# Kernel optimization log

Hardware: AMD Instinct MI355X
Metric: run time of the kernel (lower is better)

## Reference

```python
import jax, jax.numpy as jnp
import numpy as np

D_MODEL = 128
NHEAD = 8
DFF = 256
NW = 1024      # number of windows
WIN = 128      # max tokens per window
N_TOTAL = NW * WIN
NEG = -1e9


def _build_indices():
    rng = np.random.RandomState(0)
    cnt = rng.randint(WIN // 2, WIN + 1, size=NW)
    cnt_prv = rng.randint(WIN // 2, WIN + 1, size=NW)
    inds = np.concatenate([w * WIN + np.arange(c) for w, c in enumerate(cnt)]).astype(np.int64)
    inds_prv = np.concatenate([w * WIN + np.arange(c) for w, c in enumerate(cnt_prv)]).astype(np.int64)
    kpm_prv = (np.arange(WIN)[None, :] >= cnt_prv[:, None])  # True = padded key slot
    keep_inds = np.sort(rng.choice(N_TOTAL, len(inds), replace=False)).astype(np.int64)
    keep_inds_prv = np.sort(rng.choice(N_TOTAL, len(inds_prv), replace=False)).astype(np.int64)
    return inds, inds_prv, kpm_prv, keep_inds, keep_inds_prv


def setup_inputs() -> dict:
    inds, inds_prv, kpm_prv, keep_inds, keep_inds_prv = _build_indices()
    key = jax.random.key(0)
    ks = jax.random.split(key, 12)
    f = jnp.float32
    s = 0.05
    d, dff = D_MODEL, DFF
    return {
        'src': jax.random.normal(ks[0], (N_TOTAL, d), f),
        'src_prv': jax.random.normal(ks[1], (N_TOTAL, d), f),
        'pos': jax.random.normal(ks[2], (NW, WIN, d), f),
        'pos_prv': jax.random.normal(ks[3], (NW, WIN, d), f),
        'in_proj_w': jax.random.normal(ks[4], (3 * d, d), f) * s,
        'in_proj_b': jnp.zeros((3 * d,), f),
        'out_proj_w': jax.random.normal(ks[5], (d, d), f) * s,
        'out_proj_b': jnp.zeros((d,), f),
        'lin1_w': jax.random.normal(ks[6], (dff, d), f) * s,
        'lin1_b': jnp.zeros((dff,), f),
        'lin2_w': jax.random.normal(ks[7], (d, dff), f) * s,
        'lin2_b': jnp.zeros((d,), f),
        'ln1_g': jnp.ones((d,), f),
        'ln1_b': jnp.zeros((d,), f),
        'ln2_g': jnp.ones((d,), f),
        'ln2_b': jnp.zeros((d,), f),
        'keep_inds': jnp.asarray(keep_inds),
        'keep_inds_prv': jnp.asarray(keep_inds_prv),
        'inds': jnp.asarray(inds),
        'inds_prv': jnp.asarray(inds_prv),
        'key_padding_mask_prv': jnp.asarray(kpm_prv),
    }


def _layer_norm(x, g, b, eps=1e-5):
    m = x.mean(-1, keepdims=True)
    v = ((x - m) ** 2).mean(-1, keepdims=True)
    return (x - m) / jnp.sqrt(v + eps) * g + b


def reference(src, src_prv, pos, pos_prv, in_proj_w, in_proj_b, out_proj_w, out_proj_b,
              lin1_w, lin1_b, lin2_w, lin2_b, ln1_g, ln1_b, ln2_g, ln2_b,
              keep_inds, keep_inds_prv, inds, inds_prv, key_padding_mask_prv):
    d, h = D_MODEL, NHEAD
    hd = d // h
    # src[keep_inds] gather, then flat2window_v2 scatter into window grid
    sel = src[keep_inds]
    sel_prv = src_prv[keep_inds_prv]
    grid = jnp.zeros((NW * WIN, d), src.dtype).at[inds].set(sel).reshape(NW, WIN, d)
    grid_prv = jnp.zeros((NW * WIN, d), src.dtype).at[inds_prv].set(sel_prv).reshape(NW, WIN, d)
    q = grid + pos
    k = grid_prv + pos_prv
    v = grid_prv
    wq, wk, wv = jnp.split(in_proj_w, 3, axis=0)
    bq, bk, bv = jnp.split(in_proj_b, 3, axis=0)
    qh = (q @ wq.T + bq).reshape(NW, WIN, h, hd)
    kh = (k @ wk.T + bk).reshape(NW, WIN, h, hd)
    vh = (v @ wv.T + bv).reshape(NW, WIN, h, hd)
    scores = jnp.einsum('nqhd,nkhd->nhqk', qh, kh) / np.sqrt(hd).astype(np.float32)
    scores = jnp.where(key_padding_mask_prv[:, None, None, :], NEG, scores)
    attn = jax.nn.softmax(scores, axis=-1)
    out = jnp.einsum('nhqk,nkhd->nqhd', attn, vh).reshape(NW, WIN, d)
    out = out @ out_proj_w.T + out_proj_b
    # window2flat_v2 gather back, residual add at kept positions
    out_sel = out.reshape(NW * WIN, d)[inds]
    src = src.at[keep_inds].add(out_sel)  # dropout1 is identity in eval
    src = _layer_norm(src, ln1_g, ln1_b)
    ff = jax.nn.relu(src @ lin1_w.T + lin1_b) @ lin2_w.T + lin2_b
    src = _layer_norm(src + ff, ln2_g, ln2_b)
    return src
```

## Files before the change

### kernel.cpp

```cpp
#include <hip/hip_runtime.h>

#define NWIN 1024
#define WIN 128
#define DM 128
#define NTOT (NWIN*WIN)

typedef __bf16 bf16;
typedef __bf16 bf16x2 __attribute__((ext_vector_type(2)));
typedef __bf16 bf16x4 __attribute__((ext_vector_type(4)));
typedef __bf16 bf16x8 __attribute__((ext_vector_type(8)));
typedef float f32x4 __attribute__((ext_vector_type(4)));
typedef float f32x16 __attribute__((ext_vector_type(16)));

#define MFMA16(a,b,c) __builtin_amdgcn_mfma_f32_16x16x32_bf16(a,b,c,0,0,0)
#define MFMA32(a,b,c) __builtin_amdgcn_mfma_f32_32x32x16_bf16(a,b,c,0,0,0)

#define QSCALE 0.36067376022224085f


__global__ void k_prep1(const float* __restrict__ inproj, const float* __restrict__ outproj,
                        const float* __restrict__ w1, const float* __restrict__ w2,
                        bf16* __restrict__ whi,
                        int* __restrict__ mq, int* __restrict__ mkv, int* __restrict__ flag) {
    int i = blockIdx.x * 256 + threadIdx.x;
    if (i == 0) *flag = 0;
    float v;
    if (i < 49152)       v = inproj[i];
    else if (i < 65536)  v = outproj[i - 49152];
    else if (i < 98304)  v = w1[i - 65536];
    else                 v = w2[i - 98304];
    if (i < 16384) v *= QSCALE;
    whi[i] = (bf16)v;
    mq[i] = -1; mkv[i] = -1;
}

__global__ void k_prep2(const int* __restrict__ kpm_i, int* __restrict__ flag,
                        const int* __restrict__ inds, const int* __restrict__ keep, int n,
                        const int* __restrict__ inds_p, const int* __restrict__ keep_p, int np,
                        int* __restrict__ mq, int* __restrict__ mkv) {
    int j = blockIdx.x * 256 + threadIdx.x;
    if (j < 32768) {
        int v = kpm_i[j];
        if (v != 0 && v != 1) atomicOr(flag, 1);
    }
    if (j < n)  mq[inds[j]]    = keep[j];
    if (j < np) mkv[inds_p[j]] = keep_p[j];
}

__global__ void k_prep3(const int* __restrict__ kpm_i, const unsigned char* __restrict__ kpm_b,
                        const int* __restrict__ flag, unsigned char* __restrict__ kmask,
                        const float4* __restrict__ s, float4* __restrict__ d, int n4) {
    int i = blockIdx.x * 256 + threadIdx.x;
    if (i < 131072) {
        int byte_mode = *flag;
        kmask[i] = byte_mode ? (kpm_b[i] != 0) : (kpm_i[i] != 0);
    }
    int stride = gridDim.x * 256;
    for (int k = i; k < n4; k += stride) d[k] = s[k];
}

__device__ __forceinline__ void proj1p(const bf16* __restrict__ Xh,
                                       const bf16* __restrict__ WH,
                                       int l15, int g16, f32x4 acc[8]) {
    #pragma unroll
    for (int ks = 0; ks < 4; ks++) {
        bf16x8 ah = *(const bf16x8*)(Xh + l15 * 136 + ks*32 + g16*8);
        #pragma unroll
        for (int tn = 0; tn < 8; tn++) {
            bf16x8 bh = *(const bf16x8*)(WH + (size_t)(16*tn + l15) * DM + ks*32 + g16*8);
            acc[tn] = MFMA16(ah, bh, acc[tn]);
        }
    }
}

__global__ __launch_bounds__(256, 4) void k_qkv(
    const float* __restrict__ src, const float* __restrict__ src_prv,
    const float* __restrict__ pos, const float* __restrict__ pos_prv,
    const bf16* __restrict__ whi,
    const float* __restrict__ bqkv,
    const int* __restrict__ mq, const int* __restrict__ mkv,
    bf16* __restrict__ Qg, bf16* __restrict__ Kg, bf16* __restrict__ Vtg)
{
    const int blk = blockIdx.x;
    const int role = blockIdx.y;
    const int rbase = blk * 64;
    const int w = blk >> 1;
    const int kb = (blk & 1) * 64;
    const int tid = threadIdx.x;
    const int lane = tid & 63, wv = tid >> 6;
    const int l15 = lane & 15, g16 = lane >> 4;
    __shared__ bf16 X[64*136];
    __shared__ bf16 Bb[9216];

    const int srow = tid >> 2, sq4 = tid & 3;
    const int p = rbase + srow;

    if (role == 0) {
        const int g = mq[p];
        float4 a[8];
        const float4* pr = (const float4*)(pos + (size_t)p * DM + sq4 * 32);
        #pragma unroll
        for (int i = 0; i < 8; i++) a[i] = pr[i];
        if (g >= 0) {
            const float4* sr = (const float4*)(src + (size_t)g * DM + sq4 * 32);
            #pragma unroll
            for (int i = 0; i < 8; i++) {
                float4 s4 = sr[i];
                a[i].x += s4.x; a[i].y += s4.y; a[i].z += s4.z; a[i].w += s4.w;
            }
        }
        bf16* xh = X + srow * 136 + sq4 * 32;
        #pragma unroll
        for (int i = 0; i < 8; i++) {
            bf16x4 h = { (bf16)a[i].x, (bf16)a[i].y, (bf16)a[i].z, (bf16)a[i].w };
            *(bf16x4*)(xh + i * 4) = h;
        }
    } else {
        const int g = mkv[p];
        float4 a[8];
        if (role == 2) {
            const float4* pr = (const float4*)(pos_prv + (size_t)p * DM + sq4 * 32);
            #pragma unroll
            for (int i = 0; i < 8; i++) a[i] = pr[i];
        } else {
            #pragma unroll
            for (int i = 0; i < 8; i++) a[i] = make_float4(0.f, 0.f, 0.f, 0.f);
        }
        if (g >= 0) {
            const float4* sr = (const float4*)(src_prv + (size_t)g * DM + sq4 * 32);
            #pragma unroll
            for (int i = 0; i < 8; i++) {
                float4 s4 = sr[i];
                a[i].x += s4.x; a[i].y += s4.y; a[i].z += s4.z; a[i].w += s4.w;
            }
        }
        bf16* xh = X + srow * 136 + sq4 * 32;
        #pragma unroll
        for (int i = 0; i < 8; i++) {
            bf16x4 h = { (bf16)a[i].x, (bf16)a[i].y, (bf16)a[i].z, (bf16)a[i].w };
            *(bf16x4*)(xh + i * 4) = h;
        }
    }
    __syncthreads();

    const bf16* W = whi + (role == 0 ? 0 : (role == 1 ? 256*DM : 128*DM));
    f32x4 acc[8];
    for (int tn = 0; tn < 8; tn++) acc[tn] = {};
    proj1p(X + 16*wv*136, W, l15, g16, acc);

    if (role == 1) {
        #pragma unroll
        for (int tn = 0; tn < 8; tn++) {
            float bias = bqkv[256 + 16*tn + l15];
            int dim = 16*tn + l15;
            bf16x4 b = { (bf16)(acc[tn][0] + bias), (bf16)(acc[tn][1] + bias),
                         (bf16)(acc[tn][2] + bias), (bf16)(acc[tn][3] + bias) };
            *(bf16x4*)(Bb + dim * 72 + 16*wv + 4*g16) = b;
        }
        __syncthreads();
        #pragma unroll
        for (int it = 0; it < 4; it++) {
            int c = it * 256 + tid;
            int dim = c >> 3, off = (c & 7) * 8;
            *(bf16x8*)(Vtg + ((size_t)w * 128 + dim) * 128 + kb + off) = *(const bf16x8*)(Bb + dim*72 + off);
        }
    } else {
        const float bsc  = (role == 0) ? QSCALE : 1.f;
        const int   boff = (role == 0) ? 0 : 128;
        #pragma unroll
        for (int tn = 0; tn < 8; tn++) {
            float bias = bqkv[boff + 16*tn + l15] * bsc;
            #pragma unroll
            for (int r = 0; r < 4; r++)
                Bb[(16*wv + 4*g16 + r) * 136 + 16*tn + l15] = (bf16)(acc[tn][r] + bias);
        }
        __syncthreads();
        bf16* dst = (role == 0) ? Qg : Kg;
        #pragma unroll
        for (int it = 0; it < 4; it++) {
            int c = it * 256 + tid;
            int row = c >> 4, off = (c & 15) * 8;
            *(bf16x8*)(dst + (size_t)(rbase + row) * DM + off) = *(const bf16x8*)(Bb + row*136 + off);
        }
    }
}

__global__ __launch_bounds__(256) void k_attn(
    const bf16* __restrict__ Qg, const bf16* __restrict__ Kg, const bf16* __restrict__ Vtg,
    const bf16* __restrict__ whi, const float* __restrict__ ob,
    const unsigned char* __restrict__ kmask, const int* __restrict__ mq,
    float* __restrict__ x1)
{
    const int w = blockIdx.x;
    const int tid = threadIdx.x;
    const int lane = tid & 63, wv = tid >> 6;
    const int l15 = lane & 15, g16 = lane >> 4;
    const int l31 = lane & 31, h32 = lane >> 5;
    __shared__ bf16 P[4][32 * 136];
    bf16* myP = &P[wv][0];

    float mval[4];
    #pragma unroll
    for (int kt = 0; kt < 4; kt++) mval[kt] = kmask[w * WIN + 32*kt + l31] ? -1e9f : 0.f;

    const bf16* Qw = Qg + (size_t)w * WIN * DM;
    const bf16* Kw = Kg + (size_t)w * WIN * DM;
    const bf16* Vw = Vtg + (size_t)w * WIN * DM;

    f32x4 oacc[8][2];
    for (int h = 0; h < 8; h++) { oacc[h][0] = {}; oacc[h][1] = {}; }

    #pragma unroll
    for (int h = 0; h < 8; h++) {
        bf16x8 qf = *(const bf16x8*)(Qw + (size_t)(32*wv + l31) * DM + 16*h + h32*8);
        f32x16 s[4];
        #pragma unroll
        for (int kt = 0; kt < 4; kt++) {
            bf16x8 kf = *(const bf16x8*)(Kw + (size_t)(32*kt + l31) * DM + 16*h + h32*8);
            f32x16 z = {};
            s[kt] = MFMA32(qf, kf, z);
        }
        #pragma unroll
        for (int r = 0; r < 16; r++) {
            float s0 = s[0][r] + mval[0];
            float s1 = s[1][r] + mval[1];
            float s2 = s[2][r] + mval[2];
            float s3 = s[3][r] + mval[3];
            float m = fmaxf(fmaxf(s0, s1), fmaxf(s2, s3));
            #pragma unroll
            for (int d = 1; d <= 16; d <<= 1) m = fmaxf(m, __shfl_xor(m, d));
            float e0 = exp2f(s0 - m), e1 = exp2f(s1 - m);
            float e2 = exp2f(s2 - m), e3 = exp2f(s3 - m);
            float sum = e0 + e1 + e2 + e3;
            #pragma unroll
            for (int d = 1; d <= 16; d <<= 1) sum += __shfl_xor(sum, d);
            float inv = __builtin_amdgcn_rcpf(sum);
            int qrow = (r & 3) + 8 * (r >> 2) + 4 * h32;
            myP[qrow * 136 +      l31] = (bf16)(e0 * inv);
            myP[qrow * 136 + 32 + l31] = (bf16)(e1 * inv);
            myP[qrow * 136 + 64 + l31] = (bf16)(e2 * inv);
            myP[qrow * 136 + 96 + l31] = (bf16)(e3 * inv);
        }
        #pragma unroll
        for (int ks = 0; ks < 4; ks++) {
            bf16x8 p0 = *(const bf16x8*)(myP + (l15     ) * 136 + ks*32 + g16*8);
            bf16x8 p1 = *(const bf16x8*)(myP + (16 + l15) * 136 + ks*32 + g16*8);
            bf16x8 vf = *(const bf16x8*)(Vw + (size_t)(16*h + l15) * DM + ks*32 + g16*8);
            oacc[h][0] = MFMA16(p0, vf, oacc[h][0]);
            oacc[h][1] = MFMA16(p1, vf, oacc[h][1]);
        }
    }

    #pragma unroll
    for (int h = 0; h < 8; h++) {
        #pragma unroll
        for (int tq = 0; tq < 2; tq++) {
            #pragma unroll
            for (int r = 0; r < 4; r++)
                myP[(16*tq + 4*g16 + r) * 136 + 16*h + l15] = (bf16)oacc[h][tq][r];
        }
    }

    const bf16* Woh = whi + 49152;
    f32x4 oc[2][8];
    for (int tq = 0; tq < 2; tq++)
        for (int tn = 0; tn < 8; tn++)
            oc[tq][tn] = {};
    #pragma unroll
    for (int ks = 0; ks < 4; ks++) {
        bf16x8 a0 = *(const bf16x8*)(myP + (l15     ) * 136 + ks*32 + g16*8);
        bf16x8 a1 = *(const bf16x8*)(myP + (16 + l15) * 136 + ks*32 + g16*8);
        #pragma unroll
        for (int tn = 0; tn < 8; tn++) {
            bf16x8 bh = *(const bf16x8*)(Woh + (size_t)(16*tn + l15) * DM + ks*32 + g16*8);
            oc[0][tn] = MFMA16(a0, bh, oc[0][tn]);
            oc[1][tn] = MFMA16(a1, bh, oc[1][tn]);
        }
    }

    float obv[8];
    #pragma unroll
    for (int tn = 0; tn < 8; tn++) obv[tn] = ob[16*tn + l15];
    #pragma unroll
    for (int tq = 0; tq < 2; tq++) {
        #pragma unroll
        for (int r = 0; r < 4; r++) {
            int qrow = 32*wv + 16*tq + 4*g16 + r;
            int g = mq[w * WIN + qrow];
            if (g < 0) continue;
            float* orow = x1 + (size_t)g * DM;
            #pragma unroll
            for (int tn = 0; tn < 8; tn++)
                orow[16*tn + l15] += oc[tq][tn][r] + obv[tn];
        }
    }
}

__global__ __launch_bounds__(256, 4) void k_ffn(
    const float* __restrict__ x1, const bf16* __restrict__ whi,
    const float* __restrict__ g1, const float* __restrict__ b1ln,
    const float* __restrict__ fb1, const float* __restrict__ fb2,
    const float* __restrict__ g2, const float* __restrict__ b2ln,
    float* __restrict__ out)
{
    const int tid = threadIdx.x;
    const int lane = tid & 63, wv = tid >> 6;
    const int l15 = lane & 15, g16 = lane >> 4;
    const int rbase = blockIdx.x * 64 + wv * 16;
    __shared__ bf16 Hb[4][16 * 264];
    bf16* myH = &Hb[wv][0];
    const bf16* W1h = whi + 65536;
    const bf16* W2h = whi + 98304;

    float xv[4][8];
    float sum = 0.f, sq = 0.f;
    const float* xrow = x1 + (size_t)(rbase + l15) * DM;
    #pragma unroll
    for (int ks = 0; ks < 4; ks++) {
        float4 a = *(const float4*)(xrow + ks*32 + g16*8);
        float4 b = *(const float4*)(xrow + ks*32 + g16*8 + 4);
        xv[ks][0]=a.x; xv[ks][1]=a.y; xv[ks][2]=a.z; xv[ks][3]=a.w;
        xv[ks][4]=b.x; xv[ks][5]=b.y; xv[ks][6]=b.z; xv[ks][7]=b.w;
        sum += a.x+a.y+a.z+a.w + b.x+b.y+b.z+b.w;
        sq  += a.x*a.x+a.y*a.y+a.z*a.z+a.w*a.w + b.x*b.x+b.y*b.y+b.z*b.z+b.w*b.w;
    }
    sum += __shfl_xor(sum, 16); sum += __shfl_xor(sum, 32);
    sq  += __shfl_xor(sq, 16);  sq  += __shfl_xor(sq, 32);
    float mean = sum * (1.f/128.f);
    float var  = sq * (1.f/128.f) - mean * mean;
    float rstd = rsqrtf(var + 1e-5f);

    bf16x8 ah[4];
    #pragma unroll
    for (int ks = 0; ks < 4; ks++) {
        #pragma unroll
        for (int j = 0; j < 8; j++) {
            int col = ks*32 + g16*8 + j;
            float y = (xv[ks][j] - mean) * rstd * g1[col] + b1ln[col];
            ah[ks][j] = (bf16)y;
        }
    }

    #pragma unroll
    for (int c = 0; c < 2; c++) {
        f32x4 h1[8];
        #pragma unroll
        for (int t = 0; t < 8; t++) h1[t] = {};
        #pragma unroll
        for (int ks = 0; ks < 4; ks++) {
            #pragma unroll
            for (int t = 0; t < 8; t++) {
                bf16x8 bh = *(const bf16x8*)(W1h + (size_t)(16*(8*c + t) + l15) * DM + ks*32 + g16*8);
                h1[t] = MFMA16(ah[ks], bh, h1[t]);
            }
        }
        #pragma unroll
        for (int t = 0; t < 8; t++) {
            int tn = 8*c + t;
            float bias = fb1[16*tn + l15];
            #pragma unroll
            for (int r = 0; r < 4; r++) {
                float v = fmaxf(h1[t][r] + bias, 0.f);
                myH[(4*g16 + r) * 264 + 16*tn + l15] = (bf16)v;
            }
        }
    }

    f32x4 o[8];
    #pragma unroll
    for (int tn = 0; tn < 8; tn++) o[tn] = {};
    #pragma unroll
    for (int ks = 0; ks < 8; ks++) {
        bf16x8 a = *(const bf16x8*)(myH + l15 * 264 + ks*32 + g16*8);
        #pragma unroll
        for (int tn = 0; tn < 8; tn++) {
            bf16x8 bh = *(const bf16x8*)(W2h + (size_t)(16*tn + l15) * 256 + ks*32 + g16*8);
            o[tn] = MFMA16(a, bh, o[tn]);
        }
    }

    #pragma unroll
    for (int r = 0; r < 4; r++) {
        int rw = 4*g16 + r;
        int row = rbase + rw;
        float bm = __shfl(mean, rw);
        float br = __shfl(rstd, rw);
        float tmp[8];
        float s2 = 0.f, q2 = 0.f;
        #pragma unroll
        for (int tn = 0; tn < 8; tn++) {
            int col = 16*tn + l15;
            float xr = x1[(size_t)row * DM + col];
            float y  = (xr - bm) * br * g1[col] + b1ln[col];
            float v  = o[tn][r] + fb2[col] + y;
            tmp[tn] = v; s2 += v; q2 += v * v;
        }
        #pragma unroll
        for (int d = 1; d <= 8; d <<= 1) { s2 += __shfl_xor(s2, d); q2 += __shfl_xor(q2, d); }
        float mean2 = s2 * (1.f/128.f);
        float var2  = q2 * (1.f/128.f) - mean2 * mean2;
        float rstd2 = rsqrtf(var2 + 1e-5f);
        #pragma unroll
        for (int tn = 0; tn < 8; tn++) {
            int col = 16*tn + l15;
            out[(size_t)row * DM + col] = (tmp[tn] - mean2) * rstd2 * g2[col] + b2ln[col];
        }
    }
}

extern "C" void kernel_launch(void* const* d_in, const int* in_sizes, int n_in,
                              void* d_out, int out_size, void* d_ws, size_t ws_size,
                              hipStream_t stream)
{
    const float* src      = (const float*)d_in[0];
    const float* src_prv  = (const float*)d_in[1];
    const float* pos      = (const float*)d_in[2];
    const float* pos_prv  = (const float*)d_in[3];
    const float* inpw     = (const float*)d_in[4];
    const float* inpb     = (const float*)d_in[5];
    const float* outpw    = (const float*)d_in[6];
    const float* outpb    = (const float*)d_in[7];
    const float* l1w      = (const float*)d_in[8];
    const float* l1b      = (const float*)d_in[9];
    const float* l2w      = (const float*)d_in[10];
    const float* l2b      = (const float*)d_in[11];
    const float* ln1g     = (const float*)d_in[12];
    const float* ln1b     = (const float*)d_in[13];
    const float* ln2g     = (const float*)d_in[14];
    const float* ln2b     = (const float*)d_in[15];
    const int* keep       = (const int*)d_in[16];
    const int* keep_p     = (const int*)d_in[17];
    const int* inds       = (const int*)d_in[18];
    const int* inds_p     = (const int*)d_in[19];
    const int n_inds = in_sizes[18], n_prv = in_sizes[19];

    char* wsb = (char*)d_ws;
    bf16* whi  = (bf16*)(wsb);
    int*  mq   = (int*)(wsb + 524288);
    int*  mkv  = (int*)(wsb + 1048576);
    bf16* Qb   = (bf16*)(wsb + 1572864);
    bf16* Kb   = (bf16*)(wsb + 1572864 + 33554432);
    bf16* Vtb  = (bf16*)(wsb + 1572864 + 2u*33554432);
    unsigned char* kmask = (unsigned char*)(wsb + 1572864 + 3u*33554432);
    int* mflag = (int*)(wsb + 1572864 + 3u*33554432 + 131072);
    float* x1 = (float*)d_out;

    int mmax = n_inds > n_prv ? n_inds : n_prv;
    if (mmax < 32768) mmax = 32768;
    k_prep1<<<512, 256, 0, stream>>>(inpw, outpw, l1w, l2w, whi, mq, mkv, mflag);
    k_prep2<<<(mmax + 255) / 256, 256, 0, stream>>>((const int*)d_in[20], mflag,
                                                    inds, keep, n_inds, inds_p, keep_p, n_prv, mq, mkv);
    k_prep3<<<2048, 256, 0, stream>>>((const int*)d_in[20], (const unsigned char*)d_in[20], mflag, kmask,
                                      (const float4*)src, (float4*)x1, NTOT * DM / 4);
    k_qkv<<<dim3(2048, 3), 256, 0, stream>>>(src, src_prv, pos, pos_prv, whi, inpb, mq, mkv, Qb, Kb, Vtb);
    k_attn<<<NWIN, 256, 0, stream>>>(Qb, Kb, Vtb, whi, outpb, kmask, mq, x1);
    k_ffn<<<NTOT / 64, 256, 0, stream>>>(x1, whi, ln1g, ln1b, l1b, l2b, ln2g, ln2b, (float*)d_out);
}
```

Measured before the change: 456.0 us.

## Replace src copy and scatter-add with bf16 attention output and inverse-index gather in FFN

Instead of copying src into the output buffer and scatter-adding fp32 attention results into it, attention now writes a dense bf16 output tensor per window. The FFN kernel gathers that output through a new inverse index map and adds it to src on the fly. This removes a full fp32 copy pass and the read-modify-write scatter. The qkv kernel also shares one LDS buffer to allow higher occupancy. In exchange the residual is rounded to bf16 and the FFN does extra indirect reads, including an uncoalesced per-element reread in the epilogue.

```diff
diff --git a/kernel.cpp b/kernel.cpp
--- a/kernel.cpp
+++ b/kernel.cpp
@@ -6,7 +6,6 @@
 #define NTOT (NWIN*WIN)
 
 typedef __bf16 bf16;
-typedef __bf16 bf16x2 __attribute__((ext_vector_type(2)));
 typedef __bf16 bf16x4 __attribute__((ext_vector_type(4)));
 typedef __bf16 bf16x8 __attribute__((ext_vector_type(8)));
 typedef float f32x4 __attribute__((ext_vector_type(4)));
@@ -21,7 +20,8 @@
 __global__ void k_prep1(const float* __restrict__ inproj, const float* __restrict__ outproj,
                         const float* __restrict__ w1, const float* __restrict__ w2,
                         bf16* __restrict__ whi,
-                        int* __restrict__ mq, int* __restrict__ mkv, int* __restrict__ flag) {
+                        int* __restrict__ mq, int* __restrict__ mkv, int* __restrict__ im,
+                        int* __restrict__ flag) {
     int i = blockIdx.x * 256 + threadIdx.x;
     if (i == 0) *flag = 0;
     float v;
@@ -31,32 +31,27 @@
     else                 v = w2[i - 98304];
     if (i < 16384) v *= QSCALE;
     whi[i] = (bf16)v;
-    mq[i] = -1; mkv[i] = -1;
+    mq[i] = -1; mkv[i] = -1; im[i] = -1;
 }
 
 __global__ void k_prep2(const int* __restrict__ kpm_i, int* __restrict__ flag,
                         const int* __restrict__ inds, const int* __restrict__ keep, int n,
                         const int* __restrict__ inds_p, const int* __restrict__ keep_p, int np,
-                        int* __restrict__ mq, int* __restrict__ mkv) {
+                        int* __restrict__ mq, int* __restrict__ mkv, int* __restrict__ im) {
     int j = blockIdx.x * 256 + threadIdx.x;
     if (j < 32768) {
         int v = kpm_i[j];
         if (v != 0 && v != 1) atomicOr(flag, 1);
     }
-    if (j < n)  mq[inds[j]]    = keep[j];
+    if (j < n)  { mq[inds[j]] = keep[j]; im[keep[j]] = inds[j]; }
     if (j < np) mkv[inds_p[j]] = keep_p[j];
 }
 
 __global__ void k_prep3(const int* __restrict__ kpm_i, const unsigned char* __restrict__ kpm_b,
-                        const int* __restrict__ flag, unsigned char* __restrict__ kmask,
-                        const float4* __restrict__ s, float4* __restrict__ d, int n4) {
+                        const int* __restrict__ flag, unsigned char* __restrict__ kmask) {
     int i = blockIdx.x * 256 + threadIdx.x;
-    if (i < 131072) {
-        int byte_mode = *flag;
-        kmask[i] = byte_mode ? (kpm_b[i] != 0) : (kpm_i[i] != 0);
-    }
-    int stride = gridDim.x * 256;
-    for (int k = i; k < n4; k += stride) d[k] = s[k];
+    int byte_mode = *flag;
+    kmask[i] = byte_mode ? (kpm_b[i] != 0) : (kpm_i[i] != 0);
 }
 
 __device__ __forceinline__ void proj1p(const bf16* __restrict__ Xh,
@@ -73,7 +68,7 @@
     }
 }
 
-__global__ __launch_bounds__(256, 4) void k_qkv(
+__global__ __launch_bounds__(256, 6) void k_qkv(
     const float* __restrict__ src, const float* __restrict__ src_prv,
     const float* __restrict__ pos, const float* __restrict__ pos_prv,
     const bf16* __restrict__ whi,
@@ -89,64 +84,59 @@
     const int tid = threadIdx.x;
     const int lane = tid & 63, wv = tid >> 6;
     const int l15 = lane & 15, g16 = lane >> 4;
-    __shared__ bf16 X[64*136];
-    __shared__ bf16 Bb[9216];
+    __shared__ bf16 S[9216];
 
     const int srow = tid >> 2, sq4 = tid & 3;
     const int p = rbase + srow;
 
-    if (role == 0) {
-        const int g = mq[p];
+    {
         float4 a[8];
-        const float4* pr = (const float4*)(pos + (size_t)p * DM + sq4 * 32);
-        #pragma unroll
-        for (int i = 0; i < 8; i++) a[i] = pr[i];
-        if (g >= 0) {
-            const float4* sr = (const float4*)(src + (size_t)g * DM + sq4 * 32);
-            #pragma unroll
-            for (int i = 0; i < 8; i++) {
-                float4 s4 = sr[i];
-                a[i].x += s4.x; a[i].y += s4.y; a[i].z += s4.z; a[i].w += s4.w;
+        if (role == 0) {
+            const int g = mq[p];
+            const float4* pr = (const float4*)(pos + (size_t)p * DM + sq4 * 32);
+            #pragma unroll
+            for (int i = 0; i < 8; i++) a[i] = pr[i];
+            if (g >= 0) {
+                const float4* sr = (const float4*)(src + (size_t)g * DM + sq4 * 32);
+                #pragma unroll
+                for (int i = 0; i < 8; i++) {
+                    float4 s4 = sr[i];
+                    a[i].x += s4.x; a[i].y += s4.y; a[i].z += s4.z; a[i].w += s4.w;
+                }
             }
-        }
-        bf16* xh = X + srow * 136 + sq4 * 32;
+        } else {
+            const int g = mkv[p];
+            if (role == 2) {
+                const float4* pr = (const float4*)(pos_prv + (size_t)p * DM + sq4 * 32);
+                #pragma unroll
+                for (int i = 0; i < 8; i++) a[i] = pr[i];
+            } else {
+                #pragma unroll
+                for (int i = 0; i < 8; i++) a[i] = make_float4(0.f, 0.f, 0.f, 0.f);
+            }
+            if (g >= 0) {
+                const float4* sr = (const float4*)(src_prv + (size_t)g * DM + sq4 * 32);
+                #pragma unroll
+                for (int i = 0; i < 8; i++) {
+                    float4 s4 = sr[i];
+                    a[i].x += s4.x; a[i].y += s4.y; a[i].z += s4.z; a[i].w += s4.w;
+                }
+            }
+        }
+        bf16* xh = S + srow * 136 + sq4 * 32;
         #pragma unroll
         for (int i = 0; i < 8; i++) {
             bf16x4 h = { (bf16)a[i].x, (bf16)a[i].y, (bf16)a[i].z, (bf16)a[i].w };
             *(bf16x4*)(xh + i * 4) = h;
         }
-    } else {
-        const int g = mkv[p];
-        float4 a[8];
-        if (role == 2) {
-            const float4* pr = (const float4*)(pos_prv + (size_t)p * DM + sq4 * 32);
-            #pragma unroll
-            for (int i = 0; i < 8; i++) a[i] = pr[i];
-        } else {
-            #pragma unroll
-            for (int i = 0; i < 8; i++) a[i] = make_float4(0.f, 0.f, 0.f, 0.f);
-        }
-        if (g >= 0) {
-            const float4* sr = (const float4*)(src_prv + (size_t)g * DM + sq4 * 32);
-            #pragma unroll
-            for (int i = 0; i < 8; i++) {
-                float4 s4 = sr[i];
-                a[i].x += s4.x; a[i].y += s4.y; a[i].z += s4.z; a[i].w += s4.w;
-            }
-        }
-        bf16* xh = X + srow * 136 + sq4 * 32;
-        #pragma unroll
-        for (int i = 0; i < 8; i++) {
-            bf16x4 h = { (bf16)a[i].x, (bf16)a[i].y, (bf16)a[i].z, (bf16)a[i].w };
-            *(bf16x4*)(xh + i * 4) = h;
-        }
     }
     __syncthreads();
 
     const bf16* W = whi + (role == 0 ? 0 : (role == 1 ? 256*DM : 128*DM));
     f32x4 acc[8];
     for (int tn = 0; tn < 8; tn++) acc[tn] = {};
-    proj1p(X + 16*wv*136, W, l15, g16, acc);
+    proj1p(S + 16*wv*136, W, l15, g16, acc);
+    __syncthreads();
 
     if (role == 1) {
         #pragma unroll
@@ -155,14 +145,14 @@
             int dim = 16*tn + l15;
             bf16x4 b = { (bf16)(acc[tn][0] + bias), (bf16)(acc[tn][1] + bias),
                          (bf16)(acc[tn][2] + bias), (bf16)(acc[tn][3] + bias) };
-            *(bf16x4*)(Bb + dim * 72 + 16*wv + 4*g16) = b;
+            *(bf16x4*)(S + dim * 72 + 16*wv + 4*g16) = b;
         }
         __syncthreads();
         #pragma unroll
         for (int it = 0; it < 4; it++) {
             int c = it * 256 + tid;
             int dim = c >> 3, off = (c & 7) * 8;
-            *(bf16x8*)(Vtg + ((size_t)w * 128 + dim) * 128 + kb + off) = *(const bf16x8*)(Bb + dim*72 + off);
+            *(bf16x8*)(Vtg + ((size_t)w * 128 + dim) * 128 + kb + off) = *(const bf16x8*)(S + dim*72 + off);
         }
     } else {
         const float bsc  = (role == 0) ? QSCALE : 1.f;
@@ -172,7 +162,7 @@
             float bias = bqkv[boff + 16*tn + l15] * bsc;
             #pragma unroll
             for (int r = 0; r < 4; r++)
-                Bb[(16*wv + 4*g16 + r) * 136 + 16*tn + l15] = (bf16)(acc[tn][r] + bias);
+                S[(16*wv + 4*g16 + r) * 136 + 16*tn + l15] = (bf16)(acc[tn][r] + bias);
         }
         __syncthreads();
         bf16* dst = (role == 0) ? Qg : Kg;
@@ -180,7 +170,7 @@
         for (int it = 0; it < 4; it++) {
             int c = it * 256 + tid;
             int row = c >> 4, off = (c & 15) * 8;
-            *(bf16x8*)(dst + (size_t)(rbase + row) * DM + off) = *(const bf16x8*)(Bb + row*136 + off);
+            *(bf16x8*)(dst + (size_t)(rbase + row) * DM + off) = *(const bf16x8*)(S + row*136 + off);
         }
     }
 }
@@ -188,8 +178,8 @@
 __global__ __launch_bounds__(256) void k_attn(
     const bf16* __restrict__ Qg, const bf16* __restrict__ Kg, const bf16* __restrict__ Vtg,
     const bf16* __restrict__ whi, const float* __restrict__ ob,
-    const unsigned char* __restrict__ kmask, const int* __restrict__ mq,
-    float* __restrict__ x1)
+    const unsigned char* __restrict__ kmask,
+    bf16* __restrict__ Ob)
 {
     const int w = blockIdx.x;
     const int tid = threadIdx.x;
@@ -284,20 +274,25 @@
     #pragma unroll
     for (int tq = 0; tq < 2; tq++) {
         #pragma unroll
-        for (int r = 0; r < 4; r++) {
-            int qrow = 32*wv + 16*tq + 4*g16 + r;
-            int g = mq[w * WIN + qrow];
-            if (g < 0) continue;
-            float* orow = x1 + (size_t)g * DM;
-            #pragma unroll
-            for (int tn = 0; tn < 8; tn++)
-                orow[16*tn + l15] += oc[tq][tn][r] + obv[tn];
-        }
+        for (int tn = 0; tn < 8; tn++) {
+            #pragma unroll
+            for (int r = 0; r < 4; r++)
+                myP[(16*tq + 4*g16 + r) * 136 + 16*tn + l15] = (bf16)(oc[tq][tn][r] + obv[tn]);
+        }
+    }
+    __syncthreads();
+    bf16* Orow = Ob + ((size_t)w * 128 + 32*wv) * DM;
+    #pragma unroll
+    for (int it = 0; it < 8; it++) {
+        int c = it * 64 + lane;
+        int row = c >> 4, off = (c & 15) * 8;
+        *(bf16x8*)(Orow + (size_t)row * DM + off) = *(const bf16x8*)(myP + row*136 + off);
     }
 }
 
 __global__ __launch_bounds__(256, 4) void k_ffn(
-    const float* __restrict__ x1, const bf16* __restrict__ whi,
+    const float* __restrict__ src, const bf16* __restrict__ Ob, const int* __restrict__ im,
+    const bf16* __restrict__ whi,
     const float* __restrict__ g1, const float* __restrict__ b1ln,
     const float* __restrict__ fb1, const float* __restrict__ fb2,
     const float* __restrict__ g2, const float* __restrict__ b2ln,
@@ -312,17 +307,25 @@
     const bf16* W1h = whi + 65536;
     const bf16* W2h = whi + 98304;
 
+    const int myrow = rbase + l15;
+    const int imr = im[myrow];
     float xv[4][8];
     float sum = 0.f, sq = 0.f;
-    const float* xrow = x1 + (size_t)(rbase + l15) * DM;
+    const float* xrow = src + (size_t)myrow * DM;
+    const bf16* orow = Ob + (size_t)(imr < 0 ? 0 : imr) * DM;
     #pragma unroll
     for (int ks = 0; ks < 4; ks++) {
         float4 a = *(const float4*)(xrow + ks*32 + g16*8);
         float4 b = *(const float4*)(xrow + ks*32 + g16*8 + 4);
         xv[ks][0]=a.x; xv[ks][1]=a.y; xv[ks][2]=a.z; xv[ks][3]=a.w;
         xv[ks][4]=b.x; xv[ks][5]=b.y; xv[ks][6]=b.z; xv[ks][7]=b.w;
-        sum += a.x+a.y+a.z+a.w + b.x+b.y+b.z+b.w;
-        sq  += a.x*a.x+a.y*a.y+a.z*a.z+a.w*a.w + b.x*b.x+b.y*b.y+b.z*b.z+b.w*b.w;
+        if (imr >= 0) {
+            bf16x8 ov = *(const bf16x8*)(orow + ks*32 + g16*8);
+            #pragma unroll
+            for (int j = 0; j < 8; j++) xv[ks][j] = xv[ks][j] + (float)ov[j];
+        }
+        #pragma unroll
+        for (int j = 0; j < 8; j++) { sum += xv[ks][j]; sq += xv[ks][j]*xv[ks][j]; }
     }
     sum += __shfl_xor(sum, 16); sum += __shfl_xor(sum, 32);
     sq  += __shfl_xor(sq, 16);  sq  += __shfl_xor(sq, 32);
@@ -385,12 +388,14 @@
         int row = rbase + rw;
         float bm = __shfl(mean, rw);
         float br = __shfl(rstd, rw);
+        int imr2 = __shfl(imr, rw);
         float tmp[8];
         float s2 = 0.f, q2 = 0.f;
         #pragma unroll
         for (int tn = 0; tn < 8; tn++) {
             int col = 16*tn + l15;
-            float xr = x1[(size_t)row * DM + col];
+            float xr = src[(size_t)row * DM + col];
+            if (imr2 >= 0) xr = xr + (float)Ob[(size_t)imr2 * DM + col];
             float y  = (xr - bm) * br * g1[col] + b1ln[col];
             float v  = o[tn][r] + fb2[col] + y;
             tmp[tn] = v; s2 += v; q2 += v * v;
@@ -438,21 +443,21 @@
     bf16* whi  = (bf16*)(wsb);
     int*  mq   = (int*)(wsb + 524288);
     int*  mkv  = (int*)(wsb + 1048576);
-    bf16* Qb   = (bf16*)(wsb + 1572864);
-    bf16* Kb   = (bf16*)(wsb + 1572864 + 33554432);
-    bf16* Vtb  = (bf16*)(wsb + 1572864 + 2u*33554432);
-    unsigned char* kmask = (unsigned char*)(wsb + 1572864 + 3u*33554432);
-    int* mflag = (int*)(wsb + 1572864 + 3u*33554432 + 131072);
-    float* x1 = (float*)d_out;
+    int*  im   = (int*)(wsb + 1572864);
+    bf16* Qb   = (bf16*)(wsb + 2097152);
+    bf16* Kb   = (bf16*)(wsb + 2097152 + 1u*33554432);
+    bf16* Vtb  = (bf16*)(wsb + 2097152 + 2u*33554432);
+    bf16* Ob   = (bf16*)(wsb + 2097152 + 3u*33554432);
+    unsigned char* kmask = (unsigned char*)(wsb + 2097152 + 4u*33554432);
+    int* mflag = (int*)(wsb + 2097152 + 4u*33554432 + 131072);
 
     int mmax = n_inds > n_prv ? n_inds : n_prv;
     if (mmax < 32768) mmax = 32768;
-    k_prep1<<<512, 256, 0, stream>>>(inpw, outpw, l1w, l2w, whi, mq, mkv, mflag);
+    k_prep1<<<512, 256, 0, stream>>>(inpw, outpw, l1w, l2w, whi, mq, mkv, im, mflag);
     k_prep2<<<(mmax + 255) / 256, 256, 0, stream>>>((const int*)d_in[20], mflag,
-                                                    inds, keep, n_inds, inds_p, keep_p, n_prv, mq, mkv);
-    k_prep3<<<2048, 256, 0, stream>>>((const int*)d_in[20], (const unsigned char*)d_in[20], mflag, kmask,
-                                      (const float4*)src, (float4*)x1, NTOT * DM / 4);
+                                                    inds, keep, n_inds, inds_p, keep_p, n_prv, mq, mkv, im);
+    k_prep3<<<512, 256, 0, stream>>>((const int*)d_in[20], (const unsigned char*)d_in[20], mflag, kmask);
     k_qkv<<<dim3(2048, 3), 256, 0, stream>>>(src, src_prv, pos, pos_prv, whi, inpb, mq, mkv, Qb, Kb, Vtb);
-    k_attn<<<NWIN, 256, 0, stream>>>(Qb, Kb, Vtb, whi, outpb, kmask, mq, x1);
-    k_ffn<<<NTOT / 64, 256, 0, stream>>>(x1, whi, ln1g, ln1b, l1b, l2b, ln2g, ln2b, (float*)d_out);
-}
+    k_attn<<<NWIN, 256, 0, stream>>>(Qb, Kb, Vtb, whi, outpb, kmask, Ob);
+    k_ffn<<<NTOT / 64, 256, 0, stream>>>(src, Ob, im, whi, ln1g, ln1b, l1b, l2b, ln2g, ln2b, (float*)d_out);
+}
```

New measurement: 441.1 us. -3.3%, faster.
